# Kernel optimization log

Hardware: AMD Instinct MI355X
Metric: run time of the kernel (lower is better)

## Reference

```python
import jax, jax.numpy as jnp
import numpy as np
import math
from jax import lax

ROT = math.radians(45.0)   # rotation_range in radians
TR = 1.0                   # translation_range
P = 50                     # n_particles
ITERS = 30                 # n_iterations
SUB = 256                  # fitness_subsample
MU = P // 2
C_SIGMA = 0.3
D_SIGMA = 1.0


def axis_angle_to_R(a):
    # a: [..., 3] -> [..., 3, 3] via Rodrigues' formula
    theta = jnp.linalg.norm(a, axis=-1, keepdims=True)
    axis = a / (theta + 1e-8)
    x, y, z = axis[..., 0], axis[..., 1], axis[..., 2]
    o = jnp.zeros_like(x)
    K = jnp.stack([jnp.stack([o, -z, y], -1),
                   jnp.stack([z, o, -x], -1),
                   jnp.stack([-y, x, o], -1)], -2)
    th = theta[..., None]
    I = jnp.eye(3, dtype=a.dtype)
    return I + jnp.sin(th) * K + (1.0 - jnp.cos(th)) * (K @ K)


def chamfer(x, y):
    # x: [M,S,3], y: [M,T,3] -> [M]; symmetric chamfer on squared NN distances
    d2 = (jnp.sum(x * x, -1)[:, :, None] + jnp.sum(y * y, -1)[:, None, :]
          - 2.0 * jnp.einsum('msd,mtd->mst', x, y))
    return jnp.min(d2, axis=2).mean(axis=1) + jnp.min(d2, axis=1).mean(axis=1)


def evaluate(src, tgt, positions):
    # src [B,S,3], tgt [B,T,3], positions [B,Pn,6] -> fitness [B,Pn]
    B, Pn, _ = positions.shape
    R = axis_angle_to_R(positions[..., :3])            # [B,Pn,3,3]
    t = positions[..., 3:]
    transformed = jnp.einsum('bnj,bpkj->bpnk', src, R) + t[:, :, None, :]
    x = transformed.reshape(B * Pn, -1, 3)
    y = jnp.broadcast_to(tgt[:, None], (B, Pn) + tgt.shape[1:]).reshape(B * Pn, -1, 3)
    return chamfer(x, y).reshape(B, Pn)


def clamp6(v):
    return jnp.concatenate([jnp.clip(v[..., :3], -ROT, ROT),
                            jnp.clip(v[..., 3:], -TR, TR)], axis=-1)


def run_cmaes(source, target, key):
    B, N, _ = source.shape
    M = target.shape[1]
    S = min(SUB, N)
    k1, k2, k3 = jax.random.split(key, 3)
    src = source[:, jax.random.permutation(k1, N)[:S], :] if S < N else source
    tgt = target[:, jax.random.permutation(k2, M)[:S], :] if S < M else target

    mean = jnp.zeros((B, 6), jnp.float32)
    sigma = jnp.concatenate([jnp.full((B, 3), ROT * 0.3, jnp.float32),
                             jnp.full((B, 3), TR * 0.3, jnp.float32)], axis=1)
    w = np.log(MU + 0.5) - np.log(np.arange(1, MU + 1))
    w = jnp.asarray(w / w.sum(), jnp.float32)       # [MU] recombination weights
    gbest_pos = mean
    gbest_fit = jnp.full((B,), jnp.inf, jnp.float32)

    def step(carry, k):
        mean, sigma, gbest_pos, gbest_fit = carry
        z = jax.random.normal(k, (B, P, 6), jnp.float32)
        off = clamp6(mean[:, None] + sigma[:, None] * z)        # [B,P,6]
        fit = evaluate(src, tgt, off)                            # [B,P]
        order = jnp.argsort(fit, axis=1)
        pidx = order[:, :MU]
        pz = jnp.take_along_axis(z, pidx[..., None], axis=1)     # [B,MU,6]
        ppos = jnp.take_along_axis(off, pidx[..., None], axis=1)
        mean_new = jnp.einsum('m,bmd->bd', w, ppos)
        mean_z = jnp.einsum('m,bmd->bd', w, pz)
        s = sigma * jnp.exp(C_SIGMA / D_SIGMA * (jnp.mean(jnp.abs(mean_z), -1, keepdims=True) - 1.0))
        s = jnp.concatenate([jnp.clip(s[:, :3], ROT * 0.01, ROT * 0.5),
                             jnp.clip(s[:, 3:], TR * 0.01, TR * 0.5)], axis=1)
        best_fit = jnp.take_along_axis(fit, order[:, :1], axis=1)[:, 0]
        best_pos = jnp.take_along_axis(off, order[:, :1, None], axis=1)[:, 0]
        impr = best_fit < gbest_fit
        gbest_pos = jnp.where(impr[:, None], best_pos, gbest_pos)
        gbest_fit = jnp.where(impr, best_fit, gbest_fit)
        return (mean_new, s, gbest_pos, gbest_fit), None

    keys = jax.random.split(k3, ITERS)
    (mean, sigma, gbest_pos, gbest_fit), _ = lax.scan(step, (mean, sigma, gbest_pos, gbest_fit), keys)

    mean_fit = evaluate(src, tgt, mean[:, None, :])[:, 0]
    gbest_pos = jnp.where((mean_fit < gbest_fit)[:, None], mean, gbest_pos)
    return gbest_pos


def _forward(source, target):
    # Optimization runs under no_grad in the original -> stop_gradient here
    gbest = lax.stop_gradient(run_cmaes(source, target, jax.random.key(42)))
    R = axis_angle_to_R(gbest[:, :3])          # [B,3,3]
    t = gbest[:, 3:]                            # [B,3]
    aligned = jnp.einsum('bnj,bkj->bnk', source, R) + t[:, None, :]
    return R, t, aligned


def setup_inputs() -> dict:
    key = jax.random.key(0)
    k1, k2 = jax.random.split(key)
    source = jax.random.normal(k1, (32, 16384, 3), jnp.float32)
    target = jax.random.normal(k2, (32, 16384, 3), jnp.float32)
    return {"source": source, "target": target}


def reference(source, target):
    return _forward(source, target)
```

## Files before the change

### kernel.cpp

```cpp
#include <hip/hip_runtime.h>
#include <stdint.h>
#include <math.h>

#define NB 32
#define NPTS 16384
#define SS 256
#define POPP 50
#define MUU 25
#define NITERS 30

#define ROTF  ((float)0.7853981633974483)
#define SIG0R ((float)(0.7853981633974483*0.3))
#define SIG0T ((float)0.3)
#define SLOR  ((float)(0.7853981633974483*0.01))
#define SHIR  ((float)(0.7853981633974483*0.5))
#define SLOT  ((float)0.01)
#define SHIT  ((float)0.5)
#define SQRT2F ((float)1.4142135623730951)
#define ULOW  (-0.99999994f)

__host__ __device__ inline uint32_t rotl32(uint32_t v, int n){ return (v<<n)|(v>>(32-n)); }

__host__ __device__ inline void tf2x32(uint32_t k0, uint32_t k1, uint32_t x0, uint32_t x1,
                                       uint32_t &o0, uint32_t &o1){
  uint32_t ks2 = k0 ^ k1 ^ 0x1BD11BDAu;
  x0 += k0; x1 += k1;
#define TFR(r) { x0 += x1; x1 = rotl32(x1, r); x1 ^= x0; }
  TFR(13) TFR(15) TFR(26) TFR(6)
  x0 += k1; x1 += ks2 + 1u;
  TFR(17) TFR(29) TFR(16) TFR(24)
  x0 += ks2; x1 += k0 + 2u;
  TFR(13) TFR(15) TFR(26) TFR(6)
  x0 += k0; x1 += k1 + 3u;
  TFR(17) TFR(29) TFR(16) TFR(24)
  x0 += k1; x1 += ks2 + 4u;
  TFR(13) TFR(15) TFR(26) TFR(6)
  x0 += ks2; x1 += k0 + 5u;
#undef TFR
  o0 = x0; o1 = x1;
}

__device__ inline float erfinv32(float x){
  float w = -log1pf(-x*x);
  float p;
  if (w < 5.0f) {
    w = w - 2.5f;
    p = 2.81022636e-08f;
    p = fmaf(p, w, 3.43273939e-07f);
    p = fmaf(p, w, -3.5233877e-06f);
    p = fmaf(p, w, -4.39150654e-06f);
    p = fmaf(p, w, 0.00021858087f);
    p = fmaf(p, w, -0.00125372503f);
    p = fmaf(p, w, -0.00417768164f);
    p = fmaf(p, w, 0.246640727f);
    p = fmaf(p, w, 1.50140941f);
  } else {
    w = sqrtf(w) - 3.0f;
    p = -0.000200214257f;
    p = fmaf(p, w, 0.000100950558f);
    p = fmaf(p, w, 0.00134934322f);
    p = fmaf(p, w, -0.00367342844f);
    p = fmaf(p, w, 0.00573950773f);
    p = fmaf(p, w, -0.0076224613f);
    p = fmaf(p, w, 0.00943887047f);
    p = fmaf(p, w, 1.00167406f);
    p = fmaf(p, w, 2.83297682f);
  }
  return p * x;
}

__device__ inline void axisangle_R(float ax, float ay, float az, float R[9]){
  float th = sqrtf(ax*ax + ay*ay + az*az);
  float den = th + 1e-8f;
  float ux = ax/den, uy = ay/den, uz = az/den;
  float s = sinf(th), c = cosf(th);
  float omc = 1.0f - c;
  float xx=ux*ux, yy=uy*uy, zz=uz*uz;
  float xy=ux*uy, xz=ux*uz, yz=uy*uz;
  R[0] = 1.0f + omc*(-(yy+zz));
  R[1] = s*(-uz) + omc*xy;
  R[2] = s*uy    + omc*xz;
  R[3] = s*uz    + omc*xy;
  R[4] = 1.0f + omc*(-(xx+zz));
  R[5] = s*(-ux) + omc*yz;
  R[6] = s*(-uy) + omc*xz;
  R[7] = s*ux    + omc*yz;
  R[8] = 1.0f + omc*(-(xx+yy));
}

struct WArr { float w[MUU]; };

__global__ void k_init(float* mean, float* sigma, float* gbest_pos, float* gbest_fit){
  int i = blockIdx.x*blockDim.x + threadIdx.x;
  if (i < NB*6){
    mean[i] = 0.0f;
    gbest_pos[i] = 0.0f;
    int d = i % 6;
    sigma[i] = (d < 3) ? SIG0R : SIG0T;
  }
  if (i < NB) gbest_fit[i] = INFINITY;
}

__global__ void k_genperm(uint64_t* comp, uint32_t sa0, uint32_t sa1,
                          uint32_t sb0, uint32_t sb1, int round){
  int i = blockIdx.x*blockDim.x + threadIdx.x;
  if (i >= 2*NPTS) return;
  int a = i >> 14;
  int idx = i & (NPTS-1);
  uint32_t kk0 = a ? sb0 : sa0;
  uint32_t kk1 = a ? sb1 : sa1;
  uint32_t o0,o1; tf2x32(kk0, kk1, 0u, (uint32_t)idx, o0, o1);
  uint32_t key = o0 ^ o1;
  uint64_t val = (round == 0) ? (uint64_t)idx : (comp[i] & 0x3FFFull);
  comp[i] = ((uint64_t)key << 28) | ((uint64_t)idx << 14) | val;
}

__global__ __launch_bounds__(1024) void k_sort_local(uint64_t* comp){
  __shared__ uint64_t buf[4096];
  int c = blockIdx.x;
  int base = c * 4096;
  int abase = (c & 3) * 4096;
  for (int t = threadIdx.x; t < 4096; t += 1024) buf[t] = comp[base + t];
  __syncthreads();
  for (int k = 2; k <= 4096; k <<= 1){
    for (int j = k >> 1; j > 0; j >>= 1){
      for (int idx = threadIdx.x; idx < 2048; idx += 1024){
        int i = ((idx & ~(j-1)) << 1) | (idx & (j-1));
        int pi = i | j;
        bool dir = (((abase + i) & k) == 0);
        uint64_t A = buf[i], Bv = buf[pi];
        bool sw = dir ? (A > Bv) : (A < Bv);
        if (sw){ buf[i] = Bv; buf[pi] = A; }
      }
      __syncthreads();
    }
  }
  for (int t = threadIdx.x; t < 4096; t += 1024) comp[base + t] = buf[t];
}

__global__ void k_sort_global(uint64_t* comp, int k, int j){
  int t = blockIdx.x*blockDim.x + threadIdx.x;
  if (t >= NPTS) return;
  int a = t >> 13;
  int idx = t & 8191;
  int i = ((idx & ~(j-1)) << 1) | (idx & (j-1));
  int pi = i | j;
  bool dir = ((i & k) == 0);
  uint64_t* arr = comp + (size_t)a * NPTS;
  uint64_t A = arr[i], Bv = arr[pi];
  bool sw = dir ? (A > Bv) : (A < Bv);
  if (sw){ arr[i] = Bv; arr[pi] = A; }
}

__global__ __launch_bounds__(1024) void k_sort_finish(uint64_t* comp, int k){
  __shared__ uint64_t buf[4096];
  int c = blockIdx.x;
  int base = c * 4096;
  int abase = (c & 3) * 4096;
  for (int t = threadIdx.x; t < 4096; t += 1024) buf[t] = comp[base + t];
  __syncthreads();
  for (int j = 2048; j > 0; j >>= 1){
    for (int idx = threadIdx.x; idx < 2048; idx += 1024){
      int i = ((idx & ~(j-1)) << 1) | (idx & (j-1));
      int pi = i | j;
      bool dir = (((abase + i) & k) == 0);
      uint64_t A = buf[i], Bv = buf[pi];
      bool sw = dir ? (A > Bv) : (A < Bv);
      if (sw){ buf[i] = Bv; buf[pi] = A; }
    }
    __syncthreads();
  }
  for (int t = threadIdx.x; t < 4096; t += 1024) comp[base + t] = buf[t];
}

__global__ void k_gather(const uint64_t* comp, const float* source, const float* target,
                         float* src_sub, float* tgt_sub){
  int t = blockIdx.x*blockDim.x + threadIdx.x;
  if (t >= 2*NB*SS) return;
  int a = t / (NB*SS);
  int r = t % (NB*SS);
  int b = r / SS;
  int s2 = r % SS;
  int val = (int)(comp[(size_t)a*NPTS + s2] & 0x3FFFull);
  const float* inp = a ? target : source;
  float* outp = a ? tgt_sub : src_sub;
  for (int d = 0; d < 3; ++d)
    outp[((size_t)b*SS + s2)*3 + d] = inp[((size_t)b*NPTS + val)*3 + d];
}

__global__ __launch_bounds__(256) void k_se(uint32_t ka, uint32_t kb, int it,
    float* __restrict__ mean_base, float* __restrict__ sigma_base,
    const float* __restrict__ src_sub, const float* __restrict__ tgt_sub,
    float* __restrict__ z_base, float* __restrict__ off_base,
    float* __restrict__ fit_base,
    float* __restrict__ gb_pos, float* __restrict__ gb_fit, WArr W){
  int c = blockIdx.x;
  int b = c / POPP;
  int tid = threadIdx.x;
  int wave = tid >> 6;
  int lane = tid & 63;

  int readP  = (it == 0) ? 0 : ((it-1)&1);
  int writeP = it & 1;
  const float* fitR = fit_base + readP*(NB*POPP);
  float*       fitW = fit_base + writeP*(NB*POPP);
  const float* zR   = z_base   + (size_t)readP*(NB*POPP*6);
  float*       zC   = z_base   + (size_t)writeP*(NB*POPP*6);
  const float* offR = off_base + (size_t)readP*(NB*POPP*6);
  float*       offC = off_base + (size_t)writeP*(NB*POPP*6);
  const float* sigR = sigma_base + readP*(NB*6);
  float*       sigW = sigma_base + writeP*(NB*6);
  const float* meanR = mean_base + readP*(NB*6);
  float*       meanW = mean_base + writeP*(NB*6);

  __shared__ float qmean[6], qsig[6];
  __shared__ float lfit[POPP];
  __shared__ int   order[POPP];
  __shared__ float mn[6], mzs[6];
  __shared__ float qoff[6];
  __shared__ float4 ysd[SS];
  __shared__ float4 xsd[SS];
  __shared__ float rmp[4][SS];
  __shared__ float cmp[4][SS];
  __shared__ float wpart[4];

  if (it > 0){
    if (tid < POPP) lfit[tid] = fitR[b*POPP + tid];
    __syncthreads();
    if (tid < POPP){
      float f = lfit[tid];
      int r = 0;
      for (int j = 0; j < POPP; ++j){
        float fj = lfit[j];
        r += (fj < f) || (fj == f && j < tid);
      }
      order[r] = tid;
    }
    __syncthreads();
    if (tid < 6){
      float a = 0.0f, bz = 0.0f;
      for (int m = 0; m < MUU; ++m){
        int idx = order[m];
        a  = fmaf(W.w[m], offR[((size_t)b*POPP + idx)*6 + tid], a);
        bz = fmaf(W.w[m], zR [((size_t)b*POPP + idx)*6 + tid], bz);
      }
      mn[tid] = a; mzs[tid] = bz;
    }
    __syncthreads();
    if (tid == 0){
      float avg = (((((fabsf(mzs[0])+fabsf(mzs[1]))+fabsf(mzs[2]))+fabsf(mzs[3]))+fabsf(mzs[4]))+fabsf(mzs[5])) / 6.0f;
      float e = expf(0.3f * (avg - 1.0f));
      for (int d = 0; d < 6; ++d){
        float sN = sigR[b*6 + d] * e;
        float lo = (d < 3) ? SLOR : SLOT;
        float hi = (d < 3) ? SHIR : SHIT;
        sN = fminf(fmaxf(sN, lo), hi);
        qsig[d] = sN; sigW[b*6 + d] = sN;
        qmean[d] = mn[d]; meanW[b*6 + d] = mn[d];
      }
      int i0 = order[0];
      float bf = lfit[i0];
      if (bf < gb_fit[b]){
        gb_fit[b] = bf;
        for (int d = 0; d < 6; ++d) gb_pos[b*6 + d] = offR[((size_t)b*POPP + i0)*6 + d];
      }
    }
  } else {
    if (tid < 6){ qmean[tid] = meanR[b*6 + tid]; qsig[tid] = sigR[b*6 + tid]; }
  }
  __syncthreads();

  if (tid < 6){
    int i = c*6 + tid;
    uint32_t o0,o1; tf2x32(ka, kb, 0u, (uint32_t)i, o0, o1);
    uint32_t bits = o0 ^ o1;
    float u = __uint_as_float((bits >> 9) | 0x3F800000u) - 1.0f;
    u = u * 2.0f + ULOW;
    u = fmaxf(ULOW, u);
    float zz = SQRT2F * erfinv32(u);
    float m = qmean[tid], sg = qsig[tid];
    float v = fmaf(sg, zz, m);
    float lim = (tid < 3) ? ROTF : 1.0f;
    v = fminf(fmaxf(v, -lim), lim);
    zC[i] = zz; offC[i] = v; qoff[tid] = v;
  }
  __syncthreads();

  float R[9];
  axisangle_R(qoff[0], qoff[1], qoff[2], R);
  float tx=qoff[3], ty=qoff[4], tz=qoff[5];

  {
    const float* tp = tgt_sub + ((size_t)b*SS + tid)*3;
    float Y0=tp[0], Y1=tp[1], Y2=tp[2];
    float sy = fmaf(Y2,Y2, fmaf(Y1,Y1, Y0*Y0));
    ysd[tid] = make_float4(-2.0f*Y0, -2.0f*Y1, -2.0f*Y2, sy);
  }
  {
    const float* sp = src_sub + ((size_t)b*SS + tid)*3;
    float X0=sp[0], X1=sp[1], X2=sp[2];
    float px = fmaf(X2, R[2], fmaf(X1, R[1], X0*R[0])) + tx;
    float py = fmaf(X2, R[5], fmaf(X1, R[4], X0*R[3])) + ty;
    float pz = fmaf(X2, R[8], fmaf(X1, R[7], X0*R[6])) + tz;
    float sx = fmaf(pz,pz, fmaf(py,py, px*px));
    xsd[tid] = make_float4(-2.0f*px, -2.0f*py, -2.0f*pz, sx);
  }
  __syncthreads();

  float pxj[4],pyj[4],pzj[4];
  float yxj[4],yyj[4],yzj[4];
  #pragma unroll
  for (int j = 0; j < 4; ++j){
    int i = lane + 64*j;
    float4 xv = xsd[i];
    pxj[j] = -0.5f*xv.x; pyj[j] = -0.5f*xv.y; pzj[j] = -0.5f*xv.z;
    float4 yv = ysd[i];
    yxj[j] = -0.5f*yv.x; yyj[j] = -0.5f*yv.y; yzj[j] = -0.5f*yv.z;
  }

  float rm0=INFINITY, rm1=INFINITY, rm2=INFINITY, rm3=INFINITY;
  float cm0=INFINITY, cm1=INFINITY, cm2=INFINITY, cm3=INFINITY;
  int tbeg = wave*64;
  #pragma unroll 8
  for (int t = tbeg; t < tbeg+64; ++t){
    float4 yv = ysd[t];
    float4 xv = xsd[t];
    rm0 = fminf(rm0, fmaf(pxj[0], yv.x, fmaf(pyj[0], yv.y, fmaf(pzj[0], yv.z, yv.w))));
    rm1 = fminf(rm1, fmaf(pxj[1], yv.x, fmaf(pyj[1], yv.y, fmaf(pzj[1], yv.z, yv.w))));
    rm2 = fminf(rm2, fmaf(pxj[2], yv.x, fmaf(pyj[2], yv.y, fmaf(pzj[2], yv.z, yv.w))));
    rm3 = fminf(rm3, fmaf(pxj[3], yv.x, fmaf(pyj[3], yv.y, fmaf(pzj[3], yv.z, yv.w))));
    cm0 = fminf(cm0, fmaf(yxj[0], xv.x, fmaf(yyj[0], xv.y, fmaf(yzj[0], xv.z, xv.w))));
    cm1 = fminf(cm1, fmaf(yxj[1], xv.x, fmaf(yyj[1], xv.y, fmaf(yzj[1], xv.z, xv.w))));
    cm2 = fminf(cm2, fmaf(yxj[2], xv.x, fmaf(yyj[2], xv.y, fmaf(yzj[2], xv.z, xv.w))));
    cm3 = fminf(cm3, fmaf(yxj[3], xv.x, fmaf(yyj[3], xv.y, fmaf(yzj[3], xv.z, xv.w))));
  }

  rmp[wave][lane+  0] = rm0;  cmp[wave][lane+  0] = cm0;
  rmp[wave][lane+ 64] = rm1;  cmp[wave][lane+ 64] = cm1;
  rmp[wave][lane+128] = rm2;  cmp[wave][lane+128] = cm2;
  rmp[wave][lane+192] = rm3;  cmp[wave][lane+192] = cm3;
  __syncthreads();

  float fx = xsd[tid].w + fminf(fminf(rmp[0][tid], rmp[1][tid]),
                                fminf(rmp[2][tid], rmp[3][tid]));
  float fy = ysd[tid].w + fminf(fminf(cmp[0][tid], cmp[1][tid]),
                                fminf(cmp[2][tid], cmp[3][tid]));
  float acc = fx + fy;

  for (int m = 32; m > 0; m >>= 1) acc += __shfl_xor(acc, m, 64);
  if (lane == 0) wpart[wave] = acc;
  __syncthreads();
  if (tid == 0) fitW[c] = (((wpart[0]+wpart[1])+wpart[2])+wpart[3]) * (1.0f/256.0f);
}

__global__ __launch_bounds__(128) void k_eval(const float* __restrict__ pos, int Pn,
    const float* __restrict__ src_sub, const float* __restrict__ tgt_sub,
    float* __restrict__ fit){
  int c = blockIdx.x;
  int b = c / Pn;
  int tid = threadIdx.x;
  int wave = tid >> 6;
  int lane = tid & 63;
  __shared__ float4 ysd[SS];
  __shared__ float4 xsd[SS];
  __shared__ float wpart[2];

  const float* q = pos + (size_t)c*6;
  float R[9];
  axisangle_R(q[0], q[1], q[2], R);
  float tx=q[3], ty=q[4], tz=q[5];

  for (int i = tid; i < SS; i += 128){
    const float* tp = tgt_sub + ((size_t)b*SS + i)*3;
    float Y0=tp[0], Y1=tp[1], Y2=tp[2];
    float sy = fmaf(Y2,Y2, fmaf(Y1,Y1, Y0*Y0));
    ysd[i] = make_float4(-2.0f*Y0, -2.0f*Y1, -2.0f*Y2, sy);
  }

  int xi0 = wave*128 + lane;
  int xi1 = xi0 + 64;
  float px0,py0,pz0,sx0, px1,py1,pz1,sx1;
  {
    const float* sp = src_sub + ((size_t)b*SS + xi0)*3;
    float X0=sp[0], X1=sp[1], X2=sp[2];
    px0 = fmaf(X2, R[2], fmaf(X1, R[1], X0*R[0])) + tx;
    py0 = fmaf(X2, R[5], fmaf(X1, R[4], X0*R[3])) + ty;
    pz0 = fmaf(X2, R[8], fmaf(X1, R[7], X0*R[6])) + tz;
    sx0 = fmaf(pz0,pz0, fmaf(py0,py0, px0*px0));
    xsd[xi0] = make_float4(-2.0f*px0, -2.0f*py0, -2.0f*pz0, sx0);
  }
  {
    const float* sp = src_sub + ((size_t)b*SS + xi1)*3;
    float X0=sp[0], X1=sp[1], X2=sp[2];
    px1 = fmaf(X2, R[2], fmaf(X1, R[1], X0*R[0])) + tx;
    py1 = fmaf(X2, R[5], fmaf(X1, R[4], X0*R[3])) + ty;
    pz1 = fmaf(X2, R[8], fmaf(X1, R[7], X0*R[6])) + tz;
    sx1 = fmaf(pz1,pz1, fmaf(py1,py1, px1*px1));
    xsd[xi1] = make_float4(-2.0f*px1, -2.0f*py1, -2.0f*pz1, sx1);
  }
  __syncthreads();

  float rm0 = INFINITY, rm1 = INFINITY;
  #pragma unroll 8
  for (int t = 0; t < SS; ++t){
    float4 yv = ysd[t];
    rm0 = fminf(rm0, fmaf(px0, yv.x, fmaf(py0, yv.y, fmaf(pz0, yv.z, yv.w))));
    rm1 = fminf(rm1, fmaf(px1, yv.x, fmaf(py1, yv.y, fmaf(pz1, yv.z, yv.w))));
  }
  float acc = (sx0 + rm0) + (sx1 + rm1);

  float4 yv0 = ysd[xi0];
  float4 yv1 = ysd[xi1];
  float yx0 = -0.5f*yv0.x, yy0 = -0.5f*yv0.y, yz0 = -0.5f*yv0.z, sy0 = yv0.w;
  float yx1 = -0.5f*yv1.x, yy1 = -0.5f*yv1.y, yz1 = -0.5f*yv1.z, sy1 = yv1.w;
  float cm0 = INFINITY, cm1 = INFINITY;
  #pragma unroll 8
  for (int t = 0; t < SS; ++t){
    float4 xv = xsd[t];
    cm0 = fminf(cm0, fmaf(yx0, xv.x, fmaf(yy0, xv.y, fmaf(yz0, xv.z, xv.w))));
    cm1 = fminf(cm1, fmaf(yx1, xv.x, fmaf(yy1, xv.y, fmaf(yz1, xv.z, xv.w))));
  }
  acc += (sy0 + cm0) + (sy1 + cm1);

  for (int m = 32; m > 0; m >>= 1) acc += __shfl_xor(acc, m, 64);
  if (lane == 0) wpart[wave] = acc;
  __syncthreads();
  if (tid == 0) fit[c] = (wpart[0] + wpart[1]) * (1.0f/256.0f);
}

__global__ __launch_bounds__(64) void k_update(const float* __restrict__ fit,
    const float* __restrict__ off, const float* __restrict__ z,
    float* mean, float* sigma, float* gbest_pos, float* gbest_fit, WArr W){
  int b = blockIdx.x;
  int tid = threadIdx.x;
  __shared__ float lfit[POPP];
  __shared__ int order[POPP];
  __shared__ float mn[6], mz[6];
  if (tid < POPP) lfit[tid] = fit[b*POPP + tid];
  __syncthreads();
  if (tid < POPP){
    float f = lfit[tid];
    int r = 0;
    for (int j = 0; j < POPP; ++j){
      float fj = lfit[j];
      r += (fj < f) || (fj == f && j < tid);
    }
    order[r] = tid;
  }
  __syncthreads();
  if (tid < 6){
    float a = 0.0f, bz = 0.0f;
    for (int m = 0; m < MUU; ++m){
      int idx = order[m];
      a  = fmaf(W.w[m], off[((size_t)b*POPP + idx)*6 + tid], a);
      bz = fmaf(W.w[m], z  [((size_t)b*POPP + idx)*6 + tid], bz);
    }
    mn[tid] = a; mz[tid] = bz;
  }
  __syncthreads();
  if (tid == 0){
    float avg = (((((fabsf(mz[0])+fabsf(mz[1]))+fabsf(mz[2]))+fabsf(mz[3]))+fabsf(mz[4]))+fabsf(mz[5])) / 6.0f;
    float e = expf(0.3f * (avg - 1.0f));
    for (int d = 0; d < 6; ++d){
      float sN = sigma[b*6 + d] * e;
      float lo = (d < 3) ? SLOR : SLOT;
      float hi = (d < 3) ? SHIR : SHIT;
      sN = fminf(fmaxf(sN, lo), hi);
      sigma[b*6 + d] = sN;
      mean[b*6 + d] = mn[d];
    }
    int i0 = order[0];
    float bf = lfit[i0];
    if (bf < gbest_fit[b]){
      gbest_fit[b] = bf;
      for (int d = 0; d < 6; ++d) gbest_pos[b*6 + d] = off[((size_t)b*POPP + i0)*6 + d];
    }
  }
}

__global__ void k_finalize(const float* mean, const float* mean_fit,
                           const float* gbest_pos, const float* gbest_fit, float* out){
  int b = blockIdx.x;
  if (threadIdx.x != 0) return;
  bool um = mean_fit[b] < gbest_fit[b];
  float g[6];
  for (int d = 0; d < 6; ++d) g[d] = um ? mean[b*6 + d] : gbest_pos[b*6 + d];
  float R[9];
  axisangle_R(g[0], g[1], g[2], R);
  for (int i = 0; i < 9; ++i) out[b*9 + i] = R[i];
  for (int d = 0; d < 3; ++d) out[NB*9 + b*3 + d] = g[3 + d];
}

__global__ void k_aligned(const float* __restrict__ src, const float* __restrict__ out_rt,
                          float* __restrict__ aligned){
  int idx = blockIdx.x*blockDim.x + threadIdx.x;
  if (idx >= NB*NPTS) return;
  int b = idx / NPTS;
  const float* R = out_rt + b*9;
  const float* t = out_rt + NB*9 + b*3;
  const float* p = src + (size_t)idx*3;
  float X0=p[0], X1=p[1], X2=p[2];
  float* o = aligned + (size_t)idx*3;
  o[0] = fmaf(X2, R[2], fmaf(X1, R[1], X0*R[0])) + t[0];
  o[1] = fmaf(X2, R[5], fmaf(X1, R[4], X0*R[3])) + t[1];
  o[2] = fmaf(X2, R[8], fmaf(X1, R[7], X0*R[6])) + t[2];
}

struct HKey { uint32_t a, b; };
static inline HKey h_tf(HKey k, uint32_t x0, uint32_t x1){
  uint32_t o0,o1; tf2x32(k.a, k.b, x0, x1, o0, o1);
  return {o0, o1};
}

static void run_sort(uint64_t* comp, hipStream_t stream){
  hipLaunchKernelGGL(k_sort_local,  dim3(8),  dim3(1024), 0, stream, comp);
  hipLaunchKernelGGL(k_sort_global, dim3(64), dim3(256),  0, stream, comp, 8192, 4096);
  hipLaunchKernelGGL(k_sort_finish, dim3(8),  dim3(1024), 0, stream, comp, 8192);
  hipLaunchKernelGGL(k_sort_global, dim3(64), dim3(256),  0, stream, comp, 16384, 8192);
  hipLaunchKernelGGL(k_sort_global, dim3(64), dim3(256),  0, stream, comp, 16384, 4096);
  hipLaunchKernelGGL(k_sort_finish, dim3(8),  dim3(1024), 0, stream, comp, 16384);
}

extern "C" void kernel_launch(void* const* d_in, const int* in_sizes, int n_in,
                              void* d_out, int out_size, void* d_ws, size_t ws_size,
                              hipStream_t stream){
  const float* source = (const float*)d_in[0];
  const float* target = (const float*)d_in[1];
  float* out = (float*)d_out;

  uint8_t* w = (uint8_t*)d_ws;
  size_t o = 0;
  auto alloc = [&](size_t bytes){ void* p = w + o; o += (bytes + 255) & ~(size_t)255; return p; };
  uint64_t* comp   = (uint64_t*)alloc(2*(size_t)NPTS*8);
  float* src_sub   = (float*)alloc((size_t)NB*SS*3*4);
  float* tgt_sub   = (float*)alloc((size_t)NB*SS*3*4);
  float* z_buf     = (float*)alloc(2*(size_t)NB*POPP*6*4);
  float* off_buf   = (float*)alloc(2*(size_t)NB*POPP*6*4);
  float* fit_buf   = (float*)alloc(2*(size_t)NB*POPP*4);
  float* mean_buf  = (float*)alloc(2*(size_t)NB*6*4);
  float* sigma_buf = (float*)alloc(2*(size_t)NB*6*4);
  float* gb_pos    = (float*)alloc((size_t)NB*6*4);
  float* gb_fit    = (float*)alloc((size_t)NB*4);
  float* mean_fit  = (float*)alloc((size_t)NB*4);
  (void)ws_size; (void)in_sizes; (void)n_in; (void)out_size;

  HKey key0 = {0u, 42u};
  HKey k1 = h_tf(key0, 0u, 0u);
  HKey k2 = h_tf(key0, 0u, 1u);
  HKey k3 = h_tf(key0, 0u, 2u);
  HKey srcA  = h_tf(k1, 0u, 0u);
  HKey srcS1 = h_tf(k1, 0u, 1u);
  HKey srcS2 = h_tf(srcA, 0u, 1u);
  HKey tgtA  = h_tf(k2, 0u, 0u);
  HKey tgtS1 = h_tf(k2, 0u, 1u);
  HKey tgtS2 = h_tf(tgtA, 0u, 1u);
  HKey itk[NITERS];
  for (int j = 0; j < NITERS; ++j) itk[j] = h_tf(k3, 0u, (uint32_t)j);

  WArr W;
  {
    double lw[MUU], s = 0.0;
    for (int m = 0; m < MUU; ++m){ lw[m] = log((double)MUU + 0.5) - log((double)(m+1)); s += lw[m]; }
    for (int m = 0; m < MUU; ++m) W.w[m] = (float)(lw[m] / s);
  }

  hipLaunchKernelGGL(k_init, dim3(1), dim3(256), 0, stream, mean_buf, sigma_buf, gb_pos, gb_fit);

  hipLaunchKernelGGL(k_genperm, dim3(128), dim3(256), 0, stream,
                     comp, srcS1.a, srcS1.b, tgtS1.a, tgtS1.b, 0);
  run_sort(comp, stream);
  hipLaunchKernelGGL(k_genperm, dim3(128), dim3(256), 0, stream,
                     comp, srcS2.a, srcS2.b, tgtS2.a, tgtS2.b, 1);
  run_sort(comp, stream);
  hipLaunchKernelGGL(k_gather, dim3(64), dim3(256), 0, stream,
                     comp, source, target, src_sub, tgt_sub);

  for (int it = 0; it < NITERS; ++it){
    hipLaunchKernelGGL(k_se, dim3(NB*POPP), dim3(256), 0, stream,
                       itk[it].a, itk[it].b, it, mean_buf, sigma_buf,
                       src_sub, tgt_sub, z_buf, off_buf, fit_buf,
                       gb_pos, gb_fit, W);
  }

  hipLaunchKernelGGL(k_update, dim3(NB), dim3(64), 0, stream,
                     fit_buf + NB*POPP, off_buf + (size_t)NB*POPP*6, z_buf + (size_t)NB*POPP*6,
                     mean_buf + NB*6, sigma_buf + NB*6, gb_pos, gb_fit, W);

  hipLaunchKernelGGL(k_eval, dim3(NB), dim3(128), 0, stream,
                     mean_buf + NB*6, 1, src_sub, tgt_sub, mean_fit);
  hipLaunchKernelGGL(k_finalize, dim3(NB), dim3(64), 0, stream,
                     mean_buf + NB*6, mean_fit, gb_pos, gb_fit, out);
  hipLaunchKernelGGL(k_aligned, dim3((NB*NPTS + 255)/256), dim3(256), 0, stream,
                     source, out, out + NB*9 + NB*3);
}
```

Baseline: 893.2 us.

## Replace bitonic sort permutation with bucket-histogram rank selection

Swaps the multi-launch bitonic sort used to build the random permutations for a counting approach. Keys are bucketed by their top 8 bits through a histogram, a prefix scan and an atomic scatter, and each element's rank is then found by comparing against the other members of its bucket. The second round writes only the first SS ranks it needs. This cuts the many sort passes and launches, but brings in atomics and a per-bucket quadratic compare, and bucket sizes of around 64 make that compare cheap.

```diff
diff --git a/kernel.cpp b/kernel.cpp
--- a/kernel.cpp
+++ b/kernel.cpp
@@ -101,8 +101,9 @@
   if (i < NB) gbest_fit[i] = INFINITY;
 }
 
-__global__ void k_genperm(uint64_t* comp, uint32_t sa0, uint32_t sa1,
-                          uint32_t sb0, uint32_t sb1, int round){
+
+__global__ void k_genc(uint64_t* comp, const int* __restrict__ payload,
+                       uint32_t sa0, uint32_t sa1, uint32_t sb0, uint32_t sb1, int round){
   int i = blockIdx.x*blockDim.x + threadIdx.x;
   if (i >= 2*NPTS) return;
   int a = i >> 14;
@@ -111,69 +112,54 @@
   uint32_t kk1 = a ? sb1 : sa1;
   uint32_t o0,o1; tf2x32(kk0, kk1, 0u, (uint32_t)idx, o0, o1);
   uint32_t key = o0 ^ o1;
-  uint64_t val = (round == 0) ? (uint64_t)idx : (comp[i] & 0x3FFFull);
+  uint64_t val = (round == 0) ? (uint64_t)idx : (uint64_t)payload[i];
   comp[i] = ((uint64_t)key << 28) | ((uint64_t)idx << 14) | val;
 }
 
-__global__ __launch_bounds__(1024) void k_sort_local(uint64_t* comp){
-  __shared__ uint64_t buf[4096];
-  int c = blockIdx.x;
-  int base = c * 4096;
-  int abase = (c & 3) * 4096;
-  for (int t = threadIdx.x; t < 4096; t += 1024) buf[t] = comp[base + t];
-  __syncthreads();
-  for (int k = 2; k <= 4096; k <<= 1){
-    for (int j = k >> 1; j > 0; j >>= 1){
-      for (int idx = threadIdx.x; idx < 2048; idx += 1024){
-        int i = ((idx & ~(j-1)) << 1) | (idx & (j-1));
-        int pi = i | j;
-        bool dir = (((abase + i) & k) == 0);
-        uint64_t A = buf[i], Bv = buf[pi];
-        bool sw = dir ? (A > Bv) : (A < Bv);
-        if (sw){ buf[i] = Bv; buf[pi] = A; }
-      }
-      __syncthreads();
-    }
-  }
-  for (int t = threadIdx.x; t < 4096; t += 1024) comp[base + t] = buf[t];
-}
-
-__global__ void k_sort_global(uint64_t* comp, int k, int j){
-  int t = blockIdx.x*blockDim.x + threadIdx.x;
-  if (t >= NPTS) return;
-  int a = t >> 13;
-  int idx = t & 8191;
-  int i = ((idx & ~(j-1)) << 1) | (idx & (j-1));
-  int pi = i | j;
-  bool dir = ((i & k) == 0);
-  uint64_t* arr = comp + (size_t)a * NPTS;
-  uint64_t A = arr[i], Bv = arr[pi];
-  bool sw = dir ? (A > Bv) : (A < Bv);
-  if (sw){ arr[i] = Bv; arr[pi] = A; }
-}
-
-__global__ __launch_bounds__(1024) void k_sort_finish(uint64_t* comp, int k){
-  __shared__ uint64_t buf[4096];
-  int c = blockIdx.x;
-  int base = c * 4096;
-  int abase = (c & 3) * 4096;
-  for (int t = threadIdx.x; t < 4096; t += 1024) buf[t] = comp[base + t];
-  __syncthreads();
-  for (int j = 2048; j > 0; j >>= 1){
-    for (int idx = threadIdx.x; idx < 2048; idx += 1024){
-      int i = ((idx & ~(j-1)) << 1) | (idx & (j-1));
-      int pi = i | j;
-      bool dir = (((abase + i) & k) == 0);
-      uint64_t A = buf[i], Bv = buf[pi];
-      bool sw = dir ? (A > Bv) : (A < Bv);
-      if (sw){ buf[i] = Bv; buf[pi] = A; }
-    }
-    __syncthreads();
-  }
-  for (int t = threadIdx.x; t < 4096; t += 1024) comp[base + t] = buf[t];
-}
-
-__global__ void k_gather(const uint64_t* comp, const float* source, const float* target,
+__global__ void k_hist(const uint64_t* __restrict__ comp, int* __restrict__ hist){
+  int i = blockIdx.x*blockDim.x + threadIdx.x;
+  if (i >= 2*NPTS) return;
+  int a = i >> 14;
+  int B = (int)(comp[i] >> 52);
+  atomicAdd(&hist[a*256 + B], 1);
+}
+
+__global__ void k_scan(const int* __restrict__ hist, int* __restrict__ offs){
+  int a = threadIdx.x;
+  if (blockIdx.x != 0 || a >= 2) return;
+  int s = 0;
+  for (int b = 0; b < 256; ++b){ offs[a*256 + b] = s; s += hist[a*256 + b]; }
+}
+
+__global__ void k_bscat(const uint64_t* __restrict__ comp, const int* __restrict__ offs,
+                        int* __restrict__ slot, uint64_t* __restrict__ grouped){
+  int i = blockIdx.x*blockDim.x + threadIdx.x;
+  if (i >= 2*NPTS) return;
+  int a = i >> 14;
+  uint64_t mc = comp[i];
+  int B = (int)(mc >> 52);
+  int p = offs[a*256 + B] + atomicAdd(&slot[a*256 + B], 1);
+  grouped[(size_t)a*NPTS + p] = mc;
+}
+
+__global__ void k_rank(const uint64_t* __restrict__ grouped, const int* __restrict__ offs,
+                       const int* __restrict__ hist, int* __restrict__ outp,
+                       int stride, int limit){
+  int i = blockIdx.x*blockDim.x + threadIdx.x;
+  if (i >= 2*NPTS) return;
+  int a = i >> 14;
+  int p = i & (NPTS-1);
+  uint64_t mc = grouped[(size_t)a*NPTS + p];
+  int B = (int)(mc >> 52);
+  int off = offs[a*256 + B];
+  int sz  = hist[a*256 + B];
+  int r = off;
+  for (int q = off; q < off + sz; ++q)
+    r += (grouped[(size_t)a*NPTS + q] < mc) ? 1 : 0;
+  if (r < limit) outp[a*stride + r] = (int)(mc & 0x3FFFull);
+}
+
+__global__ void k_gather(const int* __restrict__ outS, const float* source, const float* target,
                          float* src_sub, float* tgt_sub){
   int t = blockIdx.x*blockDim.x + threadIdx.x;
   if (t >= 2*NB*SS) return;
@@ -181,7 +167,7 @@
   int r = t % (NB*SS);
   int b = r / SS;
   int s2 = r % SS;
-  int val = (int)(comp[(size_t)a*NPTS + s2] & 0x3FFFull);
+  int val = outS[a*SS + s2];
   const float* inp = a ? target : source;
   float* outp = a ? tgt_sub : src_sub;
   for (int d = 0; d < 3; ++d)
@@ -512,15 +498,6 @@
   return {o0, o1};
 }
 
-static void run_sort(uint64_t* comp, hipStream_t stream){
-  hipLaunchKernelGGL(k_sort_local,  dim3(8),  dim3(1024), 0, stream, comp);
-  hipLaunchKernelGGL(k_sort_global, dim3(64), dim3(256),  0, stream, comp, 8192, 4096);
-  hipLaunchKernelGGL(k_sort_finish, dim3(8),  dim3(1024), 0, stream, comp, 8192);
-  hipLaunchKernelGGL(k_sort_global, dim3(64), dim3(256),  0, stream, comp, 16384, 8192);
-  hipLaunchKernelGGL(k_sort_global, dim3(64), dim3(256),  0, stream, comp, 16384, 4096);
-  hipLaunchKernelGGL(k_sort_finish, dim3(8),  dim3(1024), 0, stream, comp, 16384);
-}
-
 extern "C" void kernel_launch(void* const* d_in, const int* in_sizes, int n_in,
                               void* d_out, int out_size, void* d_ws, size_t ws_size,
                               hipStream_t stream){
@@ -531,7 +508,11 @@
   uint8_t* w = (uint8_t*)d_ws;
   size_t o = 0;
   auto alloc = [&](size_t bytes){ void* p = w + o; o += (bytes + 255) & ~(size_t)255; return p; };
-  uint64_t* comp   = (uint64_t*)alloc(2*(size_t)NPTS*8);
+  uint64_t* comp    = (uint64_t*)alloc(2*(size_t)NPTS*8);
+  uint64_t* grouped = (uint64_t*)alloc(2*(size_t)NPTS*8);
+  int* perm1 = (int*)alloc(2*(size_t)NPTS*4);
+  int* outS  = (int*)alloc(2*(size_t)SS*4);
+  int* hs    = (int*)alloc(6*512*4);
   float* src_sub   = (float*)alloc((size_t)NB*SS*3*4);
   float* tgt_sub   = (float*)alloc((size_t)NB*SS*3*4);
   float* z_buf     = (float*)alloc(2*(size_t)NB*POPP*6*4);
@@ -543,6 +524,13 @@
   float* gb_fit    = (float*)alloc((size_t)NB*4);
   float* mean_fit  = (float*)alloc((size_t)NB*4);
   (void)ws_size; (void)in_sizes; (void)n_in; (void)out_size;
+
+  int* hist1 = hs + 0*512;
+  int* slot1 = hs + 1*512;
+  int* hist2 = hs + 2*512;
+  int* slot2 = hs + 3*512;
+  int* offs1 = hs + 4*512;
+  int* offs2 = hs + 5*512;
 
   HKey key0 = {0u, 42u};
   HKey k1 = h_tf(key0, 0u, 0u);
@@ -564,16 +552,25 @@
     for (int m = 0; m < MUU; ++m) W.w[m] = (float)(lw[m] / s);
   }
 
+  hipMemsetAsync(hs, 0, 4*512*4, stream);
   hipLaunchKernelGGL(k_init, dim3(1), dim3(256), 0, stream, mean_buf, sigma_buf, gb_pos, gb_fit);
 
-  hipLaunchKernelGGL(k_genperm, dim3(128), dim3(256), 0, stream,
-                     comp, srcS1.a, srcS1.b, tgtS1.a, tgtS1.b, 0);
-  run_sort(comp, stream);
-  hipLaunchKernelGGL(k_genperm, dim3(128), dim3(256), 0, stream,
-                     comp, srcS2.a, srcS2.b, tgtS2.a, tgtS2.b, 1);
-  run_sort(comp, stream);
+  hipLaunchKernelGGL(k_genc,  dim3(128), dim3(256), 0, stream,
+                     comp, (const int*)nullptr, srcS1.a, srcS1.b, tgtS1.a, tgtS1.b, 0);
+  hipLaunchKernelGGL(k_hist,  dim3(128), dim3(256), 0, stream, comp, hist1);
+  hipLaunchKernelGGL(k_scan,  dim3(1),   dim3(64),  0, stream, hist1, offs1);
+  hipLaunchKernelGGL(k_bscat, dim3(128), dim3(256), 0, stream, comp, offs1, slot1, grouped);
+  hipLaunchKernelGGL(k_rank,  dim3(128), dim3(256), 0, stream, grouped, offs1, hist1, perm1, NPTS, NPTS);
+
+  hipLaunchKernelGGL(k_genc,  dim3(128), dim3(256), 0, stream,
+                     comp, perm1, srcS2.a, srcS2.b, tgtS2.a, tgtS2.b, 1);
+  hipLaunchKernelGGL(k_hist,  dim3(128), dim3(256), 0, stream, comp, hist2);
+  hipLaunchKernelGGL(k_scan,  dim3(1),   dim3(64),  0, stream, hist2, offs2);
+  hipLaunchKernelGGL(k_bscat, dim3(128), dim3(256), 0, stream, comp, offs2, slot2, grouped);
+  hipLaunchKernelGGL(k_rank,  dim3(128), dim3(256), 0, stream, grouped, offs2, hist2, outS, SS, SS);
+
   hipLaunchKernelGGL(k_gather, dim3(64), dim3(256), 0, stream,
-                     comp, source, target, src_sub, tgt_sub);
+                     outS, source, target, src_sub, tgt_sub);
 
   for (int it = 0; it < NITERS; ++it){
     hipLaunchKernelGGL(k_se, dim3(NB*POPP), dim3(256), 0, stream,
```

New measurement: 842.9 us, median of 2. -5.6%, faster.
